# Performance work log

Measured on AMD Instinct MI355X. Metric: run time of the kernel, lower is better.

The kernel has to match this reference:

```python
import jax, jax.numpy as jnp
import numpy as np

N_NODES = 20000
N_EDGES = 320000
NF = 128   # num_node_feats
EF = 32    # num_edge_feats
CF = 3     # num_coord_feats
H = 512    # hidden_dim


def setup_inputs() -> dict:
    key = jax.random.key(0)
    ks = jax.random.split(key, 20)
    s = lambda k, shape, fan_in: jax.random.normal(k, shape, jnp.float32) / np.sqrt(fan_in)
    return {
        "hfeats": jax.random.normal(ks[0], (N_NODES, NF), jnp.float32),
        "cfeats": jax.random.normal(ks[1], (N_NODES, CF), jnp.float32),
        "efeats": jax.random.normal(ks[2], (N_EDGES, EF), jnp.float32),
        "src": jax.random.randint(ks[3], (N_EDGES,), 0, N_NODES, jnp.int32),
        "dst": jax.random.randint(ks[4], (N_EDGES,), 0, N_NODES, jnp.int32),
        # node_expansion: Linear(NF, H)
        "Wn": s(ks[5], (NF, H), NF), "bn": jnp.zeros((H,), jnp.float32),
        # edge_expansion: Linear(EF, H)
        "We": s(ks[6], (EF, H), EF), "be": jnp.zeros((H,), jnp.float32),
        # coord_expansion: Linear(CF, H)
        "Wc": s(ks[7], (CF, H), CF), "bc": jnp.zeros((H,), jnp.float32),
        # combination_reduction_nfeats: Linear(H,H) -> CELU -> Linear(H,NF) -> CELU
        "Wn1": s(ks[8], (H, H), H), "bn1": jnp.zeros((H,), jnp.float32),
        "Wn2": s(ks[9], (H, NF), H), "bn2": jnp.zeros((NF,), jnp.float32),
        # combination_reduction_efeats: Linear(H, EF) -> CELU
        "Weo": s(ks[10], (H, EF), H), "beo": jnp.zeros((EF,), jnp.float32),
        # combination_reduction_cfeats: Linear(H, CF) -> CELU
        "Wco": s(ks[11], (H, CF), H), "bco": jnp.zeros((CF,), jnp.float32),
    }


def reference(hfeats, cfeats, efeats, src, dst,
              Wn, bn, We, be, Wc, bc,
              Wn1, bn1, Wn2, bn2, Weo, beo, Wco, bco):
    celu = jax.nn.celu
    n_nodes = hfeats.shape[0]
    # Feature expansions (Linear + CELU)
    h = celu(hfeats @ Wn + bn)   # [N, H]
    e = celu(efeats @ We + be)   # [E, H]
    c = celu(cfeats @ Wc + bc)   # [N, H]
    # edge_udf: x = |c_dst - c_src| * (h_src * e)   -> [E, H]
    x = jnp.abs(c[dst] - c[src]) * (h[src] * e)
    # update_all(copy_e, sum): scatter-sum edge messages to dst nodes
    k = jax.ops.segment_sum(x, dst, num_segments=n_nodes)  # [N, H]
    # Residual combination-reductions
    h_out = hfeats + celu(celu(k @ Wn1 + bn1) @ Wn2 + bn2)
    e_out = efeats + celu(e @ Weo + beo)
    c_out = cfeats + celu(c @ Wco + bco)
    return (h_out, c_out, e_out)
```

## Files before the change

### kernel.cpp

```cpp
#include <hip/hip_runtime.h>
#include <hip/hip_bf16.h>

#define NF 128
#define EF 32
#define CF 3
#define H  512
#define EB 32

typedef __attribute__((ext_vector_type(8))) short bf16x8;
typedef __attribute__((ext_vector_type(4))) float f32x4;

__device__ __forceinline__ float celu_f(float x) {
    return fmaxf(x, __expf(fminf(x, 0.0f)) - 1.0f);
}
__device__ __forceinline__ uint cvtpk(float lo, float hi) {
    uint r;
    asm("v_cvt_pk_bf16_f32 %0, %1, %2" : "=v"(r) : "v"(lo), "v"(hi));
    return r;
}
__device__ __forceinline__ bf16x8 pack8(float4 v0, float4 v1) {
    union { uint4 u; bf16x8 b; } r;
    r.u.x = cvtpk(v0.x, v0.y); r.u.y = cvtpk(v0.z, v0.w);
    r.u.z = cvtpk(v1.x, v1.y); r.u.w = cvtpk(v1.z, v1.w);
    return r.b;
}
__device__ __forceinline__ float b2f(ushort s) {
    union { uint u; float f; } v; v.u = ((uint)s) << 16; return v.f;
}
__device__ __forceinline__ void unpack4(uint2 v, float* o) {
    union { uint u; float f; } x;
    x.u = v.x << 16;          o[0] = x.f;
    x.u = v.x & 0xffff0000u;  o[1] = x.f;
    x.u = v.y << 16;          o[2] = x.f;
    x.u = v.y & 0xffff0000u;  o[3] = x.f;
}

__global__ void hist_kernel(const int* __restrict__ dst, int* __restrict__ cnt, int n_edges) {
    int i = blockIdx.x * 256 + threadIdx.x;
    if (i < n_edges) atomicAdd(&cnt[dst[i]], 1);
}

__global__ void scan_kernel(int* __restrict__ cnt, int n_nodes) {
    __shared__ int part[1024];
    const int t = threadIdx.x;
    const int per = (n_nodes + 1023) / 1024;
    int s = 0;
    for (int i = 0; i < per; ++i) {
        int idx = t * per + i;
        if (idx < n_nodes) s += cnt[idx];
    }
    part[t] = s;
    __syncthreads();
    for (int off = 1; off < 1024; off <<= 1) {
        int v = (t >= off) ? part[t - off] : 0;
        __syncthreads();
        part[t] += v;
        __syncthreads();
    }
    int acc = part[t] - s;
    for (int i = 0; i < per; ++i) {
        int idx = t * per + i;
        if (idx < n_nodes) {
            int c = cnt[idx];
            cnt[idx] = acc;
            acc += c;
        }
    }
}

__global__ void scatter_kernel(const int* __restrict__ dst, int* __restrict__ cursor,
                               int* __restrict__ perm, int n_edges) {
    int i = blockIdx.x * 256 + threadIdx.x;
    if (i < n_edges) {
        int pos = atomicAdd(&cursor[dst[i]], 1);
        perm[pos] = i;
    }
}

__global__ void prep_kernel(const float* __restrict__ We, const float* __restrict__ Weo,
                            const float* __restrict__ Wn, const float* __restrict__ Wn1,
                            const float* __restrict__ Wn2,
                            ushort* __restrict__ Wet, ushort* __restrict__ Weot,
                            ushort* __restrict__ Wnt, ushort* __restrict__ Wn1t,
                            ushort* __restrict__ Wn2t) {
    int i = blockIdx.x * 256 + threadIdx.x;
    if (i < H * EF) {
        int j = i / EF, k = i % EF;
        Wet[i] = (ushort)cvtpk(We[(size_t)k * H + j], 0.f);
        int o = i / H, j2 = i % H;
        Weot[i] = (ushort)cvtpk(Weo[(size_t)j2 * EF + o], 0.f);
    }
    if (i < H * NF) {
        int o = i >> 7, k = i & 127;
        Wnt[i] = (ushort)cvtpk(Wn[(size_t)k * H + o], 0.f);
        int o2 = i >> 9, k2 = i & 511;
        Wn2t[i] = (ushort)cvtpk(Wn2[(size_t)k2 * NF + o2], 0.f);
    }
    if (i < H * H) {
        int o = i >> 9, k = i & 511;
        Wn1t[i] = (ushort)cvtpk(Wn1[(size_t)k * H + o], 0.f);
    }
}

__global__ __launch_bounds__(256) void node_expand_kernel(
        const float* __restrict__ hfeats, const float* __restrict__ cfeats,
        const ushort* __restrict__ Wnt, const float* __restrict__ bn,
        const float* __restrict__ Wc, const float* __restrict__ bc,
        ushort* __restrict__ hc, int n_nodes) {
    __shared__ ushort hf[32 * NF];
    __shared__ float cf[32][4];
    const int t = threadIdx.x;
    const int lane = t & 63;
    const int w = t >> 6;
    const int node0 = blockIdx.x * 32;

    for (int i = t; i < 32 * 16; i += 256) {
        int row = i >> 4, g = i & 15;
        int node = node0 + row; if (node >= n_nodes) node = n_nodes - 1;
        const float* p = hfeats + (size_t)node * NF + g * 8;
        float4 v0 = *(const float4*)p;
        float4 v1 = *(const float4*)(p + 4);
        ((bf16x8*)hf)[row * 16 + (g ^ (row & 7))] = pack8(v0, v1);
    }
    for (int i = t; i < 32 * CF; i += 256) {
        int n = i / CF, k = i % CF;
        int node = node0 + n; if (node >= n_nodes) node = n_nodes - 1;
        cf[n][k] = cfeats[(size_t)node * CF + k];
    }
    __syncthreads();

    const int ar = lane & 15;
    const int hi = lane >> 4;
    const int ak = hi * 8;

    f32x4 acc[2][8];
    #pragma unroll
    for (int nt = 0; nt < 2; ++nt)
        #pragma unroll
        for (int q = 0; q < 8; ++q) { f32x4 z = {0.f,0.f,0.f,0.f}; acc[nt][q] = z; }

    for (int kstep = 0; kstep < NF / 32; ++kstep) {
        bf16x8 nfrag[2];
        #pragma unroll
        for (int nt = 0; nt < 2; ++nt) {
            int r = nt * 16 + ar;
            int g = kstep * 4 + hi;
            nfrag[nt] = ((const bf16x8*)hf)[r * 16 + (g ^ (r & 7))];
        }
        #pragma unroll
        for (int q = 0; q < 8; ++q) {
            bf16x8 wf = *(const bf16x8*)(Wnt + (size_t)((w * 8 + q) * 16 + ar) * NF + kstep * 32 + ak);
            acc[0][q] = __builtin_amdgcn_mfma_f32_16x16x32_bf16(wf, nfrag[0], acc[0][q], 0, 0, 0);
            acc[1][q] = __builtin_amdgcn_mfma_f32_16x16x32_bf16(wf, nfrag[1], acc[1][q], 0, 0, 0);
        }
    }
    #pragma unroll
    for (int q = 0; q < 8; ++q) {
        const int jbase = (w * 8 + q) * 16 + hi * 4;
        const float4 bv = *(const float4*)(bn + jbase);
        #pragma unroll
        for (int nt = 0; nt < 2; ++nt) {
            int node = node0 + nt * 16 + ar;
            if (node < n_nodes) {
                uint2 pk;
                pk.x = cvtpk(celu_f(acc[nt][q][0] + bv.x), celu_f(acc[nt][q][1] + bv.y));
                pk.y = cvtpk(celu_f(acc[nt][q][2] + bv.z), celu_f(acc[nt][q][3] + bv.w));
                *(uint2*)(hc + (size_t)node * 1024 + (jbase >> 2) * 8) = pk;
            }
        }
    }

    for (int i = t; i < 32 * 64; i += 256) {
        int n = i >> 6, gj = i & 63;
        int node = node0 + n;
        if (node < n_nodes) {
            int j = gj * 8;
            float c0 = cf[n][0], c1 = cf[n][1], c2 = cf[n][2];
            float v[8];
            #pragma unroll
            for (int u = 0; u < 8; ++u)
                v[u] = celu_f(bc[j + u] + c0 * Wc[j + u] + c1 * Wc[H + j + u] + c2 * Wc[2 * H + j + u]);
            uint2 p0, p1;
            p0.x = cvtpk(v[0], v[1]); p0.y = cvtpk(v[2], v[3]);
            p1.x = cvtpk(v[4], v[5]); p1.y = cvtpk(v[6], v[7]);
            *(uint2*)(hc + (size_t)node * 1024 + (2 * gj) * 8 + 4) = p0;
            *(uint2*)(hc + (size_t)node * 1024 + (2 * gj + 1) * 8 + 4) = p1;
        }
    }
}

__global__ __launch_bounds__(256) void c_out_kernel(
        const float* __restrict__ cfeats, const ushort* __restrict__ hc,
        const float* __restrict__ Wco, const float* __restrict__ bco,
        float* __restrict__ c_out, int n_nodes) {
    const int t = threadIdx.x;
    const int lane = t & 63;
    const int w = t >> 6;
    const int node = blockIdx.x * 4 + w;
    if (node >= n_nodes) return;
    uint2 cv0 = *(const uint2*)(hc + (size_t)node * 1024 + (2 * lane) * 8 + 4);
    uint2 cv1 = *(const uint2*)(hc + (size_t)node * 1024 + (2 * lane + 1) * 8 + 4);
    float cv[8];
    unpack4(cv0, cv);
    unpack4(cv1, cv + 4);
    float a0 = 0.f, a1 = 0.f, a2 = 0.f;
    #pragma unroll
    for (int u = 0; u < 8; ++u) {
        int j = lane * 8 + u;
        a0 += cv[u] * Wco[j * CF + 0];
        a1 += cv[u] * Wco[j * CF + 1];
        a2 += cv[u] * Wco[j * CF + 2];
    }
    #pragma unroll
    for (int m = 32; m >= 1; m >>= 1) {
        a0 += __shfl_xor(a0, m);
        a1 += __shfl_xor(a1, m);
        a2 += __shfl_xor(a2, m);
    }
    if (lane < 3) {
        float s = (lane == 0) ? a0 : (lane == 1) ? a1 : a2;
        c_out[(size_t)node * CF + lane] = cfeats[(size_t)node * CF + lane] + celu_f(bco[lane] + s);
    }
}

__global__ __launch_bounds__(256) void edge_kernel(
        const float* __restrict__ efeats,
        const int* __restrict__ src, const int* __restrict__ dst,
        const int* __restrict__ perm,
        const ushort* __restrict__ Wet, const float* __restrict__ be,
        const ushort* __restrict__ Weot, const float* __restrict__ beo,
        const ushort* __restrict__ hc,
        float* __restrict__ k_acc, float* __restrict__ e_out, int n_edges) {
    __shared__ ushort e512[EB * 512];
    __shared__ int s_perm[EB], s_src[EB], s_dst[EB];
    const int t = threadIdx.x;
    const int lane = t & 63;
    const int w = t >> 6;

    const int nwg = gridDim.x;
    const int q = nwg >> 3, r = nwg & 7;
    const int xcd = blockIdx.x & 7, sub = blockIdx.x >> 3;
    const int bid = (xcd < r ? xcd * (q + 1) : r * (q + 1) + (xcd - r) * q) + sub;
    const int e0 = bid * EB;

    if (t < EB) {
        int e = e0 + t;
        int pe = (e < n_edges) ? perm[e] : -1;
        s_perm[t] = pe;
        s_src[t] = (pe >= 0) ? src[pe] : 0;
        s_dst[t] = (pe >= 0) ? dst[pe] : -1;
    }
    __syncthreads();

    const int ar = lane & 15;
    const int hi = lane >> 4;
    const int ak = hi * 8;

    bf16x8 efrag[2];
    #pragma unroll
    for (int et = 0; et < 2; ++et) {
        int pe = s_perm[et * 16 + ar];
        if (pe < 0) pe = 0;
        const float* p = efeats + (size_t)pe * EF + ak;
        float4 v0 = *(const float4*)p;
        float4 v1 = *(const float4*)(p + 4);
        efrag[et] = pack8(v0, v1);
    }
    bf16x8 wfrag[8];
    #pragma unroll
    for (int qq = 0; qq < 8; ++qq)
        wfrag[qq] = *(const bf16x8*)(Wet + (size_t)((w * 8 + qq) * 16 + ar) * EF + ak);
    f32x4 acc[2][8];
    #pragma unroll
    for (int et = 0; et < 2; ++et)
        #pragma unroll
        for (int qq = 0; qq < 8; ++qq) { f32x4 z = {0.f,0.f,0.f,0.f}; acc[et][qq] = z; }
    #pragma unroll
    for (int qq = 0; qq < 8; ++qq) {
        acc[0][qq] = __builtin_amdgcn_mfma_f32_16x16x32_bf16(wfrag[qq], efrag[0], acc[0][qq], 0, 0, 0);
        acc[1][qq] = __builtin_amdgcn_mfma_f32_16x16x32_bf16(wfrag[qq], efrag[1], acc[1][qq], 0, 0, 0);
    }
    #pragma unroll
    for (int qq = 0; qq < 8; ++qq) {
        const int jbase = (w * 8 + qq) * 16 + hi * 4;
        const float4 bv = *(const float4*)(be + jbase);
        #pragma unroll
        for (int et = 0; et < 2; ++et) {
            const int e_l = et * 16 + ar;
            uint2 pk;
            pk.x = cvtpk(celu_f(acc[et][qq][0] + bv.x), celu_f(acc[et][qq][1] + bv.y));
            pk.y = cvtpk(celu_f(acc[et][qq][2] + bv.z), celu_f(acc[et][qq][3] + bv.w));
            const int gs = (jbase >> 3) ^ (e_l & 7);
            *(uint2*)(&e512[e_l * 512 + gs * 8 + (jbase & 7)]) = pk;
        }
    }
    __syncthreads();

    {
        const int grp = t >> 7;
        const int ct = t & 127;
        const int j0 = ct * 4;
        const int g = j0 >> 3, go = j0 & 7;
        float a_[4];
        a_[0] = a_[1] = a_[2] = a_[3] = 0.f;
        int cur = -1;
        #pragma unroll
        for (int i = 0; i < 16; ++i) {
            const int e = grp * 16 + i;
            const int d = __builtin_amdgcn_readfirstlane(s_dst[e]);
            const int dc = (d < 0) ? 0 : d;
            const int s_ = s_src[e];
            uint4 sv = *(const uint4*)(hc + (size_t)s_ * 1024 + ct * 8);
            uint2 cdv = *(const uint2*)(hc + (size_t)dc * 1024 + ct * 8 + 4);
            uint2 ev = *(const uint2*)(&e512[e * 512 + (g ^ (e & 7)) * 8 + go]);
            if (d != cur) {
                if (cur >= 0) {
                    #pragma unroll
                    for (int u = 0; u < 4; ++u)
                        atomicAdd(&k_acc[(size_t)cur * H + j0 + u], a_[u]);
                    a_[0] = a_[1] = a_[2] = a_[3] = 0.f;
                }
                cur = d;
            }
            if (d >= 0) {
                float hs_[4], cs_[4], cd_[4], ev_[4];
                uint2 hv; hv.x = sv.x; hv.y = sv.y;
                uint2 cv; cv.x = sv.z; cv.y = sv.w;
                unpack4(hv, hs_);
                unpack4(cv, cs_);
                unpack4(cdv, cd_);
                unpack4(ev, ev_);
                #pragma unroll
                for (int u = 0; u < 4; ++u)
                    a_[u] += fabsf(cd_[u] - cs_[u]) * (hs_[u] * ev_[u]);
            }
        }
        if (cur >= 0) {
            #pragma unroll
            for (int u = 0; u < 4; ++u)
                atomicAdd(&k_acc[(size_t)cur * H + j0 + u], a_[u]);
        }
    }

    {
        const int ot = w & 1, et = w >> 1;
        bf16x8 wfragC[16];
        #pragma unroll
        for (int kt = 0; kt < 16; ++kt)
            wfragC[kt] = *(const bf16x8*)(Weot + (size_t)(ot * 16 + ar) * H + kt * 32 + ak);
        f32x4 accc = {0.f, 0.f, 0.f, 0.f};
        const int e_l = et * 16 + ar;
        #pragma unroll
        for (int kt = 0; kt < 16; ++kt) {
            const int gs = (kt * 4 + hi) ^ (e_l & 7);
            bf16x8 b = *(const bf16x8*)(&e512[e_l * 512 + gs * 8]);
            accc = __builtin_amdgcn_mfma_f32_16x16x32_bf16(wfragC[kt], b, accc, 0, 0, 0);
        }
        const int pe = s_perm[e_l];
        if (pe >= 0) {
            const int obase = ot * 16 + hi * 4;
            const float4 bo = *(const float4*)(beo + obase);
            size_t idx = (size_t)pe * EF + obase;
            float4 ef4 = *(const float4*)(efeats + idx);
            float4 o;
            o.x = ef4.x + celu_f(accc[0] + bo.x);
            o.y = ef4.y + celu_f(accc[1] + bo.y);
            o.z = ef4.z + celu_f(accc[2] + bo.z);
            o.w = ef4.w + celu_f(accc[3] + bo.w);
            *(float4*)(e_out + idx) = o;
        }
    }
}

__global__ __launch_bounds__(256) void node_out_kernel(
        const float* __restrict__ hfeats, const float* __restrict__ k_acc,
        const ushort* __restrict__ Wn1t, const float* __restrict__ bn1,
        const ushort* __restrict__ Wn2t, const float* __restrict__ bn2,
        float* __restrict__ h_out, int n_nodes) {
    __shared__ ushort kt_s[32 * H];
    const int t = threadIdx.x;
    const int lane = t & 63;
    const int w = t >> 6;
    const int node0 = blockIdx.x * 32;

    for (int i = t; i < 32 * 64; i += 256) {
        int row = i >> 6, g = i & 63;
        int node = node0 + row; if (node >= n_nodes) node = n_nodes - 1;
        const float* p = k_acc + (size_t)node * H + g * 8;
        float4 v0 = *(const float4*)p;
        float4 v1 = *(const float4*)(p + 4);
        ((bf16x8*)kt_s)[row * 64 + (g ^ (row & 7))] = pack8(v0, v1);
    }
    __syncthreads();

    const int ar = lane & 15;
    const int hi = lane >> 4;
    const int ak = hi * 8;

    f32x4 acc[2][8];
    #pragma unroll
    for (int nt = 0; nt < 2; ++nt)
        #pragma unroll
        for (int q = 0; q < 8; ++q) { f32x4 z = {0.f,0.f,0.f,0.f}; acc[nt][q] = z; }

    for (int kstep = 0; kstep < H / 32; ++kstep) {
        bf16x8 kfrag[2];
        #pragma unroll
        for (int nt = 0; nt < 2; ++nt) {
            int rr = nt * 16 + ar;
            int g = kstep * 4 + hi;
            kfrag[nt] = ((const bf16x8*)kt_s)[rr * 64 + (g ^ (rr & 7))];
        }
        #pragma unroll
        for (int q = 0; q < 8; ++q) {
            bf16x8 wf = *(const bf16x8*)(Wn1t + (size_t)((w * 8 + q) * 16 + ar) * H + kstep * 32 + ak);
            acc[0][q] = __builtin_amdgcn_mfma_f32_16x16x32_bf16(wf, kfrag[0], acc[0][q], 0, 0, 0);
            acc[1][q] = __builtin_amdgcn_mfma_f32_16x16x32_bf16(wf, kfrag[1], acc[1][q], 0, 0, 0);
        }
    }
    __syncthreads();

    #pragma unroll
    for (int q = 0; q < 8; ++q) {
        const int jbase = (w * 8 + q) * 16 + hi * 4;
        const float4 bv = *(const float4*)(bn1 + jbase);
        #pragma unroll
        for (int nt = 0; nt < 2; ++nt) {
            const int rr = nt * 16 + ar;
            uint2 pk;
            pk.x = cvtpk(celu_f(acc[nt][q][0] + bv.x), celu_f(acc[nt][q][1] + bv.y));
            pk.y = cvtpk(celu_f(acc[nt][q][2] + bv.z), celu_f(acc[nt][q][3] + bv.w));
            const int gs = (jbase >> 3) ^ (rr & 7);
            *(uint2*)(&kt_s[rr * 512 + gs * 8 + (jbase & 7)]) = pk;
        }
    }
    __syncthreads();

    f32x4 acc2[2][2];
    #pragma unroll
    for (int nt = 0; nt < 2; ++nt)
        #pragma unroll
        for (int ct = 0; ct < 2; ++ct) { f32x4 z = {0.f,0.f,0.f,0.f}; acc2[nt][ct] = z; }

    for (int kstep = 0; kstep < H / 32; ++kstep) {
        bf16x8 tfrag[2];
        #pragma unroll
        for (int nt = 0; nt < 2; ++nt) {
            int rr = nt * 16 + ar;
            int g = kstep * 4 + hi;
            tfrag[nt] = ((const bf16x8*)kt_s)[rr * 64 + (g ^ (rr & 7))];
        }
        #pragma unroll
        for (int ct = 0; ct < 2; ++ct) {
            bf16x8 wf = *(const bf16x8*)(Wn2t + (size_t)((w * 2 + ct) * 16 + ar) * H + kstep * 32 + ak);
            acc2[0][ct] = __builtin_amdgcn_mfma_f32_16x16x32_bf16(wf, tfrag[0], acc2[0][ct], 0, 0, 0);
            acc2[1][ct] = __builtin_amdgcn_mfma_f32_16x16x32_bf16(wf, tfrag[1], acc2[1][ct], 0, 0, 0);
        }
    }
    #pragma unroll
    for (int ct = 0; ct < 2; ++ct) {
        const int jbase = (w * 2 + ct) * 16 + hi * 4;
        const float4 bv = *(const float4*)(bn2 + jbase);
        #pragma unroll
        for (int nt = 0; nt < 2; ++nt) {
            const int node = node0 + nt * 16 + ar;
            if (node < n_nodes) {
                size_t idx = (size_t)node * NF + jbase;
                float4 hf4 = *(const float4*)(hfeats + idx);
                float4 o;
                o.x = hf4.x + celu_f(acc2[nt][ct][0] + bv.x);
                o.y = hf4.y + celu_f(acc2[nt][ct][1] + bv.y);
                o.z = hf4.z + celu_f(acc2[nt][ct][2] + bv.z);
                o.w = hf4.w + celu_f(acc2[nt][ct][3] + bv.w);
                *(float4*)(h_out + idx) = o;
            }
        }
    }
}

extern "C" void kernel_launch(void* const* d_in, const int* in_sizes, int n_in,
                              void* d_out, int out_size, void* d_ws, size_t ws_size,
                              hipStream_t stream) {
    const float* hfeats = (const float*)d_in[0];
    const float* cfeats = (const float*)d_in[1];
    const float* efeats = (const float*)d_in[2];
    const int*   src    = (const int*)d_in[3];
    const int*   dst    = (const int*)d_in[4];
    const float* Wn  = (const float*)d_in[5];  const float* bn  = (const float*)d_in[6];
    const float* We  = (const float*)d_in[7];  const float* be  = (const float*)d_in[8];
    const float* Wc  = (const float*)d_in[9];  const float* bc  = (const float*)d_in[10];
    const float* Wn1 = (const float*)d_in[11]; const float* bn1 = (const float*)d_in[12];
    const float* Wn2 = (const float*)d_in[13]; const float* bn2 = (const float*)d_in[14];
    const float* Weo = (const float*)d_in[15]; const float* beo = (const float*)d_in[16];
    const float* Wco = (const float*)d_in[17]; const float* bco = (const float*)d_in[18];

    const int n_nodes = in_sizes[0] / NF;
    const int n_edges = in_sizes[2] / EF;

    float*  k_buf = (float*)d_ws;
    ushort* hc    = (ushort*)(k_buf + (size_t)n_nodes * H);
    ushort* Wet   = hc + (size_t)n_nodes * H * 2;
    ushort* Weot  = Wet + (size_t)H * EF;
    ushort* Wnt   = Weot + (size_t)H * EF;
    ushort* Wn1t  = Wnt + (size_t)H * NF;
    ushort* Wn2t  = Wn1t + (size_t)H * H;
    int*    cnt   = (int*)(Wn2t + (size_t)NF * H);
    int*    perm  = cnt + n_nodes;

    float* h_out = (float*)d_out;
    float* c_out = h_out + (size_t)n_nodes * NF;
    float* e_out = c_out + (size_t)n_nodes * CF;

    hipMemsetAsync(k_buf, 0, (size_t)n_nodes * H * sizeof(float), stream);
    hipMemsetAsync(cnt, 0, (size_t)n_nodes * sizeof(int), stream);

    prep_kernel<<<(H * H + 255) / 256, 256, 0, stream>>>(
        We, Weo, Wn, Wn1, Wn2, Wet, Weot, Wnt, Wn1t, Wn2t);
    hist_kernel<<<(n_edges + 255) / 256, 256, 0, stream>>>(dst, cnt, n_edges);
    scan_kernel<<<1, 1024, 0, stream>>>(cnt, n_nodes);
    scatter_kernel<<<(n_edges + 255) / 256, 256, 0, stream>>>(dst, cnt, perm, n_edges);

    node_expand_kernel<<<(n_nodes + 31) / 32, 256, 0, stream>>>(
        hfeats, cfeats, Wnt, bn, Wc, bc, hc, n_nodes);

    c_out_kernel<<<(n_nodes + 3) / 4, 256, 0, stream>>>(
        cfeats, hc, Wco, bco, c_out, n_nodes);

    edge_kernel<<<(n_edges + EB - 1) / EB, 256, 0, stream>>>(
        efeats, src, dst, perm, Wet, be, Weot, beo, hc, k_buf, e_out, n_edges);

    node_out_kernel<<<(n_nodes + 31) / 32, 256, 0, stream>>>(
        hfeats, k_buf, Wn1t, bn1, Wn2t, bn2, h_out, n_nodes);
}
```

Before: 479.3 us.

## Process edge block in two halves with warp-specialized scatter and edge-output GEMM

The edge kernel now handles its 32 edges as two halves of 16 and keeps only a 16x512 bf16 LDS buffer, halving shared memory per block. It also holds a single accumulator set for the expansion GEMM instead of two, and loads Weo fragments inside the loop, cutting register pressure. In each half, two waves run the gather and scatter-accumulate while the other two compute the e_out projection concurrently. In exchange there are extra barriers, and only half of the threads do the scatter work at any one time.

```diff
diff --git a/kernel.cpp b/kernel.cpp
--- a/kernel.cpp
+++ b/kernel.cpp
@@ -231,7 +231,7 @@
         const ushort* __restrict__ Weot, const float* __restrict__ beo,
         const ushort* __restrict__ hc,
         float* __restrict__ k_acc, float* __restrict__ e_out, int n_edges) {
-    __shared__ ushort e512[EB * 512];
+    __shared__ ushort e512[16 * 512];
     __shared__ int s_perm[EB], s_src[EB], s_dst[EB];
     const int t = threadIdx.x;
     const int lane = t & 63;
@@ -256,119 +256,108 @@
     const int hi = lane >> 4;
     const int ak = hi * 8;
 
-    bf16x8 efrag[2];
-    #pragma unroll
-    for (int et = 0; et < 2; ++et) {
-        int pe = s_perm[et * 16 + ar];
-        if (pe < 0) pe = 0;
-        const float* p = efeats + (size_t)pe * EF + ak;
-        float4 v0 = *(const float4*)p;
-        float4 v1 = *(const float4*)(p + 4);
-        efrag[et] = pack8(v0, v1);
-    }
     bf16x8 wfrag[8];
     #pragma unroll
     for (int qq = 0; qq < 8; ++qq)
         wfrag[qq] = *(const bf16x8*)(Wet + (size_t)((w * 8 + qq) * 16 + ar) * EF + ak);
-    f32x4 acc[2][8];
-    #pragma unroll
-    for (int et = 0; et < 2; ++et)
-        #pragma unroll
-        for (int qq = 0; qq < 8; ++qq) { f32x4 z = {0.f,0.f,0.f,0.f}; acc[et][qq] = z; }
-    #pragma unroll
-    for (int qq = 0; qq < 8; ++qq) {
-        acc[0][qq] = __builtin_amdgcn_mfma_f32_16x16x32_bf16(wfrag[qq], efrag[0], acc[0][qq], 0, 0, 0);
-        acc[1][qq] = __builtin_amdgcn_mfma_f32_16x16x32_bf16(wfrag[qq], efrag[1], acc[1][qq], 0, 0, 0);
-    }
-    #pragma unroll
-    for (int qq = 0; qq < 8; ++qq) {
-        const int jbase = (w * 8 + qq) * 16 + hi * 4;
-        const float4 bv = *(const float4*)(be + jbase);
-        #pragma unroll
-        for (int et = 0; et < 2; ++et) {
-            const int e_l = et * 16 + ar;
+
+    #pragma unroll
+    for (int half = 0; half < 2; ++half) {
+        bf16x8 efrag;
+        {
+            int pe = s_perm[half * 16 + ar];
+            if (pe < 0) pe = 0;
+            const float* p = efeats + (size_t)pe * EF + ak;
+            float4 v0 = *(const float4*)p;
+            float4 v1 = *(const float4*)(p + 4);
+            efrag = pack8(v0, v1);
+        }
+        f32x4 acc[8];
+        #pragma unroll
+        for (int qq = 0; qq < 8; ++qq) { f32x4 z = {0.f,0.f,0.f,0.f}; acc[qq] = z; }
+        #pragma unroll
+        for (int qq = 0; qq < 8; ++qq)
+            acc[qq] = __builtin_amdgcn_mfma_f32_16x16x32_bf16(wfrag[qq], efrag, acc[qq], 0, 0, 0);
+        #pragma unroll
+        for (int qq = 0; qq < 8; ++qq) {
+            const int jbase = (w * 8 + qq) * 16 + hi * 4;
+            const float4 bv = *(const float4*)(be + jbase);
             uint2 pk;
-            pk.x = cvtpk(celu_f(acc[et][qq][0] + bv.x), celu_f(acc[et][qq][1] + bv.y));
-            pk.y = cvtpk(celu_f(acc[et][qq][2] + bv.z), celu_f(acc[et][qq][3] + bv.w));
-            const int gs = (jbase >> 3) ^ (e_l & 7);
-            *(uint2*)(&e512[e_l * 512 + gs * 8 + (jbase & 7)]) = pk;
-        }
-    }
-    __syncthreads();
-
-    {
-        const int grp = t >> 7;
-        const int ct = t & 127;
-        const int j0 = ct * 4;
-        const int g = j0 >> 3, go = j0 & 7;
-        float a_[4];
-        a_[0] = a_[1] = a_[2] = a_[3] = 0.f;
-        int cur = -1;
-        #pragma unroll
-        for (int i = 0; i < 16; ++i) {
-            const int e = grp * 16 + i;
-            const int d = __builtin_amdgcn_readfirstlane(s_dst[e]);
-            const int dc = (d < 0) ? 0 : d;
-            const int s_ = s_src[e];
-            uint4 sv = *(const uint4*)(hc + (size_t)s_ * 1024 + ct * 8);
-            uint2 cdv = *(const uint2*)(hc + (size_t)dc * 1024 + ct * 8 + 4);
-            uint2 ev = *(const uint2*)(&e512[e * 512 + (g ^ (e & 7)) * 8 + go]);
-            if (d != cur) {
-                if (cur >= 0) {
+            pk.x = cvtpk(celu_f(acc[qq][0] + bv.x), celu_f(acc[qq][1] + bv.y));
+            pk.y = cvtpk(celu_f(acc[qq][2] + bv.z), celu_f(acc[qq][3] + bv.w));
+            const int gs = (jbase >> 3) ^ (ar & 7);
+            *(uint2*)(&e512[ar * 512 + gs * 8 + (jbase & 7)]) = pk;
+        }
+        __syncthreads();
+
+        if ((t >> 7) == half) {
+            const int ct = t & 127;
+            const int j0 = ct * 4;
+            const int g = j0 >> 3, go = j0 & 7;
+            float a_[4];
+            a_[0] = a_[1] = a_[2] = a_[3] = 0.f;
+            int cur = -1;
+            #pragma unroll
+            for (int i = 0; i < 16; ++i) {
+                const int e = half * 16 + i;
+                const int d = __builtin_amdgcn_readfirstlane(s_dst[e]);
+                const int dc = (d < 0) ? 0 : d;
+                const int s_ = s_src[e];
+                uint4 sv = *(const uint4*)(hc + (size_t)s_ * 1024 + ct * 8);
+                uint2 cdv = *(const uint2*)(hc + (size_t)dc * 1024 + ct * 8 + 4);
+                uint2 ev = *(const uint2*)(&e512[i * 512 + (g ^ (i & 7)) * 8 + go]);
+                if (d != cur) {
+                    if (cur >= 0) {
+                        #pragma unroll
+                        for (int u = 0; u < 4; ++u)
+                            atomicAdd(&k_acc[(size_t)cur * H + j0 + u], a_[u]);
+                        a_[0] = a_[1] = a_[2] = a_[3] = 0.f;
+                    }
+                    cur = d;
+                }
+                if (d >= 0) {
+                    float hs_[4], cs_[4], cd_[4], ev_[4];
+                    uint2 hv; hv.x = sv.x; hv.y = sv.y;
+                    uint2 cv; cv.x = sv.z; cv.y = sv.w;
+                    unpack4(hv, hs_);
+                    unpack4(cv, cs_);
+                    unpack4(cdv, cd_);
+                    unpack4(ev, ev_);
                     #pragma unroll
                     for (int u = 0; u < 4; ++u)
-                        atomicAdd(&k_acc[(size_t)cur * H + j0 + u], a_[u]);
-                    a_[0] = a_[1] = a_[2] = a_[3] = 0.f;
+                        a_[u] += fabsf(cd_[u] - cs_[u]) * (hs_[u] * ev_[u]);
                 }
-                cur = d;
             }
-            if (d >= 0) {
-                float hs_[4], cs_[4], cd_[4], ev_[4];
-                uint2 hv; hv.x = sv.x; hv.y = sv.y;
-                uint2 cv; cv.x = sv.z; cv.y = sv.w;
-                unpack4(hv, hs_);
-                unpack4(cv, cs_);
-                unpack4(cdv, cd_);
-                unpack4(ev, ev_);
+            if (cur >= 0) {
                 #pragma unroll
                 for (int u = 0; u < 4; ++u)
-                    a_[u] += fabsf(cd_[u] - cs_[u]) * (hs_[u] * ev_[u]);
+                    atomicAdd(&k_acc[(size_t)cur * H + j0 + u], a_[u]);
             }
-        }
-        if (cur >= 0) {
+        } else {
+            const int ot = w & 1;
+            f32x4 accc = {0.f, 0.f, 0.f, 0.f};
             #pragma unroll
-            for (int u = 0; u < 4; ++u)
-                atomicAdd(&k_acc[(size_t)cur * H + j0 + u], a_[u]);
-        }
-    }
-
-    {
-        const int ot = w & 1, et = w >> 1;
-        bf16x8 wfragC[16];
-        #pragma unroll
-        for (int kt = 0; kt < 16; ++kt)
-            wfragC[kt] = *(const bf16x8*)(Weot + (size_t)(ot * 16 + ar) * H + kt * 32 + ak);
-        f32x4 accc = {0.f, 0.f, 0.f, 0.f};
-        const int e_l = et * 16 + ar;
-        #pragma unroll
-        for (int kt = 0; kt < 16; ++kt) {
-            const int gs = (kt * 4 + hi) ^ (e_l & 7);
-            bf16x8 b = *(const bf16x8*)(&e512[e_l * 512 + gs * 8]);
-            accc = __builtin_amdgcn_mfma_f32_16x16x32_bf16(wfragC[kt], b, accc, 0, 0, 0);
-        }
-        const int pe = s_perm[e_l];
-        if (pe >= 0) {
-            const int obase = ot * 16 + hi * 4;
-            const float4 bo = *(const float4*)(beo + obase);
-            size_t idx = (size_t)pe * EF + obase;
-            float4 ef4 = *(const float4*)(efeats + idx);
-            float4 o;
-            o.x = ef4.x + celu_f(accc[0] + bo.x);
-            o.y = ef4.y + celu_f(accc[1] + bo.y);
-            o.z = ef4.z + celu_f(accc[2] + bo.z);
-            o.w = ef4.w + celu_f(accc[3] + bo.w);
-            *(float4*)(e_out + idx) = o;
-        }
+            for (int kt = 0; kt < 16; ++kt) {
+                bf16x8 wfC = *(const bf16x8*)(Weot + (size_t)(ot * 16 + ar) * H + kt * 32 + ak);
+                const int gs = (kt * 4 + hi) ^ (ar & 7);
+                bf16x8 b = *(const bf16x8*)(&e512[ar * 512 + gs * 8]);
+                accc = __builtin_amdgcn_mfma_f32_16x16x32_bf16(wfC, b, accc, 0, 0, 0);
+            }
+            const int pe = s_perm[half * 16 + ar];
+            if (pe >= 0) {
+                const int obase = ot * 16 + hi * 4;
+                const float4 bo = *(const float4*)(beo + obase);
+                size_t idx = (size_t)pe * EF + obase;
+                float4 ef4 = *(const float4*)(efeats + idx);
+                float4 o;
+                o.x = ef4.x + celu_f(accc[0] + bo.x);
+                o.y = ef4.y + celu_f(accc[1] + bo.y);
+                o.z = ef4.z + celu_f(accc[2] + bo.z);
+                o.w = ef4.w + celu_f(accc[3] + bo.w);
+                *(float4*)(e_out + idx) = o;
+            }
+        }
+        __syncthreads();
     }
 }
 
```

Measured after the change: 499.7 us. 4.2% more time.

## Use 512-thread edge blocks with warp specialization for scatter and output GEMM

Applied to the files above, without the earlier changes.

The edge kernel moves to 512 threads per block. The expansion MFMA work is split over 8 waves, each handling 4 output column tiles and looping over the two edge tiles to cut live accumulators. After the barrier, waves 0-3 do the gather/scatter-sum into k_acc while waves 4-7 run the efeats output GEMM concurrently, streaming Weot fragments instead of holding 16 in registers. The intent is to overlap the memory-bound scatter with the MFMA output projection and to lower register pressure for higher occupancy. The cost is a larger block, and the launch bound of 512 threads with 8 blocks may force register limits.

```diff
diff --git a/kernel.cpp b/kernel.cpp
--- a/kernel.cpp
+++ b/kernel.cpp
@@ -223,7 +223,7 @@
     }
 }
 
-__global__ __launch_bounds__(256) void edge_kernel(
+__global__ __launch_bounds__(512, 8) void edge_kernel(
         const float* __restrict__ efeats,
         const int* __restrict__ src, const int* __restrict__ dst,
         const int* __restrict__ perm,
@@ -256,47 +256,44 @@
     const int hi = lane >> 4;
     const int ak = hi * 8;
 
-    bf16x8 efrag[2];
-    #pragma unroll
-    for (int et = 0; et < 2; ++et) {
-        int pe = s_perm[et * 16 + ar];
-        if (pe < 0) pe = 0;
-        const float* p = efeats + (size_t)pe * EF + ak;
-        float4 v0 = *(const float4*)p;
-        float4 v1 = *(const float4*)(p + 4);
-        efrag[et] = pack8(v0, v1);
-    }
-    bf16x8 wfrag[8];
-    #pragma unroll
-    for (int qq = 0; qq < 8; ++qq)
-        wfrag[qq] = *(const bf16x8*)(Wet + (size_t)((w * 8 + qq) * 16 + ar) * EF + ak);
-    f32x4 acc[2][8];
-    #pragma unroll
-    for (int et = 0; et < 2; ++et)
-        #pragma unroll
-        for (int qq = 0; qq < 8; ++qq) { f32x4 z = {0.f,0.f,0.f,0.f}; acc[et][qq] = z; }
-    #pragma unroll
-    for (int qq = 0; qq < 8; ++qq) {
-        acc[0][qq] = __builtin_amdgcn_mfma_f32_16x16x32_bf16(wfrag[qq], efrag[0], acc[0][qq], 0, 0, 0);
-        acc[1][qq] = __builtin_amdgcn_mfma_f32_16x16x32_bf16(wfrag[qq], efrag[1], acc[1][qq], 0, 0, 0);
-    }
-    #pragma unroll
-    for (int qq = 0; qq < 8; ++qq) {
-        const int jbase = (w * 8 + qq) * 16 + hi * 4;
-        const float4 bv = *(const float4*)(be + jbase);
+    {
+        bf16x8 wfrag[4];
+        #pragma unroll
+        for (int qq = 0; qq < 4; ++qq)
+            wfrag[qq] = *(const bf16x8*)(Wet + (size_t)((w * 4 + qq) * 16 + ar) * EF + ak);
         #pragma unroll
         for (int et = 0; et < 2; ++et) {
+            bf16x8 efrag;
+            {
+                int pe = s_perm[et * 16 + ar];
+                if (pe < 0) pe = 0;
+                const float* p = efeats + (size_t)pe * EF + ak;
+                float4 v0 = *(const float4*)p;
+                float4 v1 = *(const float4*)(p + 4);
+                efrag = pack8(v0, v1);
+            }
+            f32x4 acc[4];
+            #pragma unroll
+            for (int qq = 0; qq < 4; ++qq) { f32x4 z = {0.f,0.f,0.f,0.f}; acc[qq] = z; }
+            #pragma unroll
+            for (int qq = 0; qq < 4; ++qq)
+                acc[qq] = __builtin_amdgcn_mfma_f32_16x16x32_bf16(wfrag[qq], efrag, acc[qq], 0, 0, 0);
             const int e_l = et * 16 + ar;
-            uint2 pk;
-            pk.x = cvtpk(celu_f(acc[et][qq][0] + bv.x), celu_f(acc[et][qq][1] + bv.y));
-            pk.y = cvtpk(celu_f(acc[et][qq][2] + bv.z), celu_f(acc[et][qq][3] + bv.w));
-            const int gs = (jbase >> 3) ^ (e_l & 7);
-            *(uint2*)(&e512[e_l * 512 + gs * 8 + (jbase & 7)]) = pk;
-        }
-    }
-    __syncthreads();
-
-    {
+            #pragma unroll
+            for (int qq = 0; qq < 4; ++qq) {
+                const int jbase = (w * 4 + qq) * 16 + hi * 4;
+                const float4 bv = *(const float4*)(be + jbase);
+                uint2 pk;
+                pk.x = cvtpk(celu_f(acc[qq][0] + bv.x), celu_f(acc[qq][1] + bv.y));
+                pk.y = cvtpk(celu_f(acc[qq][2] + bv.z), celu_f(acc[qq][3] + bv.w));
+                const int gs = (jbase >> 3) ^ (e_l & 7);
+                *(uint2*)(&e512[e_l * 512 + gs * 8 + (jbase & 7)]) = pk;
+            }
+        }
+    }
+    __syncthreads();
+
+    if (w < 4) {
         const int grp = t >> 7;
         const int ct = t & 127;
         const int j0 = ct * 4;
@@ -340,21 +337,17 @@
             for (int u = 0; u < 4; ++u)
                 atomicAdd(&k_acc[(size_t)cur * H + j0 + u], a_[u]);
         }
-    }
-
-    {
-        const int ot = w & 1, et = w >> 1;
-        bf16x8 wfragC[16];
-        #pragma unroll
-        for (int kt = 0; kt < 16; ++kt)
-            wfragC[kt] = *(const bf16x8*)(Weot + (size_t)(ot * 16 + ar) * H + kt * 32 + ak);
+    } else {
+        const int wc = w - 4;
+        const int ot = wc & 1, et = wc >> 1;
+        const int e_l = et * 16 + ar;
         f32x4 accc = {0.f, 0.f, 0.f, 0.f};
-        const int e_l = et * 16 + ar;
         #pragma unroll
         for (int kt = 0; kt < 16; ++kt) {
+            bf16x8 wfC = *(const bf16x8*)(Weot + (size_t)(ot * 16 + ar) * H + kt * 32 + ak);
             const int gs = (kt * 4 + hi) ^ (e_l & 7);
             bf16x8 b = *(const bf16x8*)(&e512[e_l * 512 + gs * 8]);
-            accc = __builtin_amdgcn_mfma_f32_16x16x32_bf16(wfragC[kt], b, accc, 0, 0, 0);
+            accc = __builtin_amdgcn_mfma_f32_16x16x32_bf16(wfC, b, accc, 0, 0, 0);
         }
         const int pe = s_perm[e_l];
         if (pe >= 0) {
@@ -526,7 +519,7 @@
     c_out_kernel<<<(n_nodes + 3) / 4, 256, 0, stream>>>(
         cfeats, hc, Wco, bco, c_out, n_nodes);
 
-    edge_kernel<<<(n_edges + EB - 1) / EB, 256, 0, stream>>>(
+    edge_kernel<<<(n_edges + EB - 1) / EB, 512, 0, stream>>>(
         efeats, src, dst, perm, Wet, be, Weot, beo, hc, k_buf, e_out, n_edges);
 
     node_out_kernel<<<(n_nodes + 31) / 32, 256, 0, stream>>>(
```

After: 485.4 us. Within noise of the previous version (+1.3%).
